# Kernel optimization log

Hardware: AMD Instinct MI355X
Metric: run time of the kernel (lower is better)

The kernel has to match this reference:

```python
import jax, jax.numpy as jnp
import numpy as np

K = 7  # number of relaxed nearest neighbors (init arg k)
EXPM1_GUARD = 1e-7
LOG_HALF = float(np.log(0.5))

def log1mexp(x):
    # log(1 - exp(x)) for x <= 0, numerically stable (guard matches torch bw-path constant)
    t = x < LOG_HALF
    xa = jnp.where(t, x, -1.0)          # safe operand for log1p(-exp(.))
    xb = jnp.where(t, -1.0, x)          # safe operand for log(-expm1(.))
    ya = jnp.log1p(-jnp.exp(xa))
    yb = jnp.log(-jnp.expm1(xb) + EXPM1_GUARD)
    return jnp.where(t, ya, yb)

def setup_inputs() -> dict:
    key = jax.random.key(0)
    k1, k2, k3, k4 = jax.random.split(key, 4)
    b, n, m, o, e, f = 4, 8192, 2048, 64, 64, 128
    x = jax.random.normal(k1, (b, n, f), dtype=jnp.float32)
    xe = jax.random.normal(k2, (b, n, e), dtype=jnp.float32)
    ye = jax.random.normal(k3, (b, m, e), dtype=jnp.float32)
    log_temp_param = jnp.zeros((1,), dtype=jnp.float32)
    I = jax.random.randint(k4, (b, m, o), 0, n, dtype=jnp.int64)
    return {"x": x, "xe": xe, "ye": ye, "log_temp_param": log_temp_param, "I": I}

def reference(x, xe, ye, log_temp_param, I):
    b, n, f = x.shape
    m, o = I.shape[1], I.shape[2]
    bidx = jnp.arange(b)[:, None, None]          # [b,1,1] batch index for gathers

    # ---- compute_distances (indexed path): D[b,m,o] = -||xe[I] - ye||^2 ----
    xg_e = xe[bidx, I]                           # [b,m,o,e] gathered candidate embeddings
    diff = xg_e - ye[:, :, None, :]              # [b,m,o,e]
    D = -jnp.sum(diff * diff, axis=-1)           # [b,m,o]

    # ---- NeuralNearestNeighbors: temperature + k-step relaxed top-k ----
    temperature = jnp.exp(log_temp_param[0])     # log_temp_bias = log(1) = 0
    logits = (D / temperature).reshape(b * m, o)
    samples = []
    for _ in range(K):
        w = jax.nn.log_softmax(logits, axis=1)   # [b*m,o]
        samples.append(jnp.exp(w).reshape(b, m, o))
        logits = logits + log1mexp(w)
    W = jnp.stack(samples, axis=3)               # [b,m,o,K]

    # ---- aggregate_output: z[b,m,f,K] = sum_o W[b,m,o,K] * x[b, I[b,m,o], f] ----
    xg = x[bidx, I]                              # [b,m,o,f]
    z = jnp.einsum('bmok,bmof->bmfk', W, xg)     # [b,m,f,K]
    return z
```

## Files before the change

kernel.cpp:

```cpp
#include <hip/hip_runtime.h>
#include <math.h>

#define B_  4
#define N_  8192
#define M_  2048
#define O_  64
#define E_  64
#define F_  128
#define K_  7

__device__ __forceinline__ unsigned short f32_to_bf16_rne(float f) {
    unsigned u = __float_as_uint(f);
    u += 0x7FFFu + ((u >> 16) & 1u);
    return (unsigned short)(u >> 16);
}

__global__ __launch_bounds__(256) void x_to_bf16_kernel(
    const float* __restrict__ x, unsigned short* __restrict__ xb16)
{
    const size_t i = (size_t)blockIdx.x * 256 + threadIdx.x;
    const float4 v = ((const float4*)x)[i];
    ushort4 o;
    o.x = f32_to_bf16_rne(v.x);
    o.y = f32_to_bf16_rne(v.y);
    o.z = f32_to_bf16_rne(v.z);
    o.w = f32_to_bf16_rne(v.w);
    ((ushort4*)xb16)[i] = o;
}

__global__ __launch_bounds__(128, 6) void n3agg_kernel(
    const unsigned short* __restrict__ xb16, const float* __restrict__ xe,
    const float* __restrict__ ye, const float* __restrict__ log_temp,
    const int* __restrict__ I, float* __restrict__ out)
{
    __shared__ __align__(16) int   s_I[2][O_];
    __shared__ __align__(16) float s_ye[2][E_];
    __shared__ __align__(16) float s_W[2][O_][8];

    const int tid  = threadIdx.x;
    const int w    = tid >> 6;
    const int lane = tid & 63;
    const int bid  = blockIdx.x * 2 + w;
    const int b    = bid >> 11;

    const int my_idx = I[(size_t)bid * O_ + lane];
    s_I[w][lane]  = my_idx;
    s_ye[w][lane] = ye[(size_t)bid * E_ + lane];

    const float4* xr4 = (const float4*)(xe + ((size_t)b * N_ + my_idx) * E_);
    const float4* ye4 = (const float4*)(&s_ye[w][0]);
    float S[16];
    #pragma unroll
    for (int q = 0; q < 4; ++q) {
        float4 xa = xr4[q],      ya = ye4[q];
        float4 xb = xr4[q + 4],  yb = ye4[q + 4];
        float4 xc = xr4[q + 8],  yc = ye4[q + 8];
        float4 xd = xr4[q + 12], yd = ye4[q + 12];
        float da, db, dc, dd;

        da = __fsub_rn(xa.x, ya.x); db = __fsub_rn(xb.x, yb.x);
        dc = __fsub_rn(xc.x, yc.x); dd = __fsub_rn(xd.x, yd.x);
        S[4*q+0] = __fadd_rn(__fadd_rn(__fmul_rn(da,da), __fmul_rn(db,db)),
                             __fadd_rn(__fmul_rn(dc,dc), __fmul_rn(dd,dd)));

        da = __fsub_rn(xa.y, ya.y); db = __fsub_rn(xb.y, yb.y);
        dc = __fsub_rn(xc.y, yc.y); dd = __fsub_rn(xd.y, yd.y);
        S[4*q+1] = __fadd_rn(__fadd_rn(__fmul_rn(da,da), __fmul_rn(db,db)),
                             __fadd_rn(__fmul_rn(dc,dc), __fmul_rn(dd,dd)));

        da = __fsub_rn(xa.z, ya.z); db = __fsub_rn(xb.z, yb.z);
        dc = __fsub_rn(xc.z, yc.z); dd = __fsub_rn(xd.z, yd.z);
        S[4*q+2] = __fadd_rn(__fadd_rn(__fmul_rn(da,da), __fmul_rn(db,db)),
                             __fadd_rn(__fmul_rn(dc,dc), __fmul_rn(dd,dd)));

        da = __fsub_rn(xa.w, ya.w); db = __fsub_rn(xb.w, yb.w);
        dc = __fsub_rn(xc.w, yc.w); dd = __fsub_rn(xd.w, yd.w);
        S[4*q+3] = __fadd_rn(__fadd_rn(__fmul_rn(da,da), __fmul_rn(db,db)),
                             __fadd_rn(__fmul_rn(dc,dc), __fmul_rn(dd,dd)));
    }
    float t8[8], t4[4], t2[2], res;
    #pragma unroll
    for (int l = 0; l < 8; ++l) t8[l] = __fadd_rn(S[l], S[l + 8]);
    #pragma unroll
    for (int l = 0; l < 4; ++l) t4[l] = __fadd_rn(t8[l], t8[l + 4]);
    t2[0] = __fadd_rn(t4[0], t4[2]);
    t2[1] = __fadd_rn(t4[1], t4[3]);
    res   = __fadd_rn(t2[0], t2[1]);

    const float temp = expf(log_temp[0]);
    float logit = __fdiv_rn(-res, temp);

    float wreg[K_];
    #pragma unroll
    for (int k = 0; k < K_; ++k) {
        float mx = logit;
        #pragma unroll
        for (int d = 1; d < 64; d <<= 1) mx = fmaxf(mx, __shfl_xor(mx, d));
        float sh = __fsub_rn(logit, mx);
        float ex = expf(sh);
        float t = __fadd_rn(ex, __shfl_xor(ex, 16));
        t = __fadd_rn(t, __shfl_xor(t, 32));
        t = __fadd_rn(t, __shfl_xor(t, 8));
        t = __fadd_rn(t, __shfl_xor(t, 4));
        t = __fadd_rn(t, __shfl_xor(t, 2));
        t = __fadd_rn(t, __shfl_xor(t, 1));
        const float sm = t;

        float wv = __fsub_rn(sh, logf(sm));
        wreg[k] = expf(wv);

        float lm;
        if (wv < -0.69314718055994530942f) {
            lm = log1pf(-expf(wv));
        } else {
            lm = logf(__fadd_rn(-expm1f(wv), 1e-7f));
        }
        logit = __fadd_rn(logit, lm);
    }
    {
        float* wp = &s_W[w][lane][0];
        *(float4*)wp       = make_float4(wreg[0], wreg[1], wreg[2], wreg[3]);
        *(float2*)(wp + 4) = make_float2(wreg[4], wreg[5]);
        wp[6] = wreg[6];
    }

    const int h  = lane >> 5;
    const int fl = lane & 31;
    float acc[4][K_];
    #pragma unroll
    for (int q = 0; q < 4; ++q)
        #pragma unroll
        for (int k = 0; k < K_; ++k) acc[q][k] = 0.f;

    const unsigned short* xb = xb16 + (size_t)b * N_ * F_ + 4 * fl;
    #pragma unroll 2
    for (int t = 0; t < 32; ++t) {
        const int o = 2 * t + h;
        const int idx = s_I[w][o];
        const ushort4 xu = *(const ushort4*)(xb + (size_t)idx * F_);
        const float xv0 = __uint_as_float((unsigned)xu.x << 16);
        const float xv1 = __uint_as_float((unsigned)xu.y << 16);
        const float xv2 = __uint_as_float((unsigned)xu.z << 16);
        const float xv3 = __uint_as_float((unsigned)xu.w << 16);
        const float* wrow = &s_W[w][o][0];
        const float4 wa = *(const float4*)(wrow);
        const float4 wb = *(const float4*)(wrow + 4);
        const float wk[K_] = {wa.x, wa.y, wa.z, wa.w, wb.x, wb.y, wb.z};
        #pragma unroll
        for (int k = 0; k < K_; ++k) {
            acc[0][k] = fmaf(wk[k], xv0, acc[0][k]);
            acc[1][k] = fmaf(wk[k], xv1, acc[1][k]);
            acc[2][k] = fmaf(wk[k], xv2, acc[2][k]);
            acc[3][k] = fmaf(wk[k], xv3, acc[3][k]);
        }
    }
    #pragma unroll
    for (int q = 0; q < 4; ++q)
        #pragma unroll
        for (int k = 0; k < K_; ++k)
            acc[q][k] += __shfl_xor(acc[q][k], 32);

    if (lane < 32) {
        const float* af = &acc[0][0];
        float4* op4 = (float4*)(out + (size_t)bid * F_ * K_ + fl * 28);
        #pragma unroll
        for (int j = 0; j < 7; ++j)
            op4[j] = make_float4(af[4*j], af[4*j+1], af[4*j+2], af[4*j+3]);
    }
}

__global__ __launch_bounds__(128, 6) void n3agg_fused_f32_kernel(
    const float* __restrict__ x, const float* __restrict__ xe,
    const float* __restrict__ ye, const float* __restrict__ log_temp,
    const int* __restrict__ I, float* __restrict__ out)
{
    __shared__ __align__(16) int   s_I[2][O_];
    __shared__ __align__(16) float s_ye[2][E_];
    __shared__ __align__(16) float s_W[2][O_][8];

    const int tid  = threadIdx.x;
    const int w    = tid >> 6;
    const int lane = tid & 63;
    const int bid  = blockIdx.x * 2 + w;
    const int b    = bid >> 11;

    const int my_idx = I[(size_t)bid * O_ + lane];
    s_I[w][lane]  = my_idx;
    s_ye[w][lane] = ye[(size_t)bid * E_ + lane];

    const float4* xr4 = (const float4*)(xe + ((size_t)b * N_ + my_idx) * E_);
    const float4* ye4 = (const float4*)(&s_ye[w][0]);
    float S[16];
    #pragma unroll
    for (int q = 0; q < 4; ++q) {
        float4 xa = xr4[q],      ya = ye4[q];
        float4 xb = xr4[q + 4],  yb = ye4[q + 4];
        float4 xc = xr4[q + 8],  yc = ye4[q + 8];
        float4 xd = xr4[q + 12], yd = ye4[q + 12];
        float da, db, dc, dd;
        da = __fsub_rn(xa.x, ya.x); db = __fsub_rn(xb.x, yb.x);
        dc = __fsub_rn(xc.x, yc.x); dd = __fsub_rn(xd.x, yd.x);
        S[4*q+0] = __fadd_rn(__fadd_rn(__fmul_rn(da,da), __fmul_rn(db,db)),
                             __fadd_rn(__fmul_rn(dc,dc), __fmul_rn(dd,dd)));
        da = __fsub_rn(xa.y, ya.y); db = __fsub_rn(xb.y, yb.y);
        dc = __fsub_rn(xc.y, yc.y); dd = __fsub_rn(xd.y, yd.y);
        S[4*q+1] = __fadd_rn(__fadd_rn(__fmul_rn(da,da), __fmul_rn(db,db)),
                             __fadd_rn(__fmul_rn(dc,dc), __fmul_rn(dd,dd)));
        da = __fsub_rn(xa.z, ya.z); db = __fsub_rn(xb.z, yb.z);
        dc = __fsub_rn(xc.z, yc.z); dd = __fsub_rn(xd.z, yd.z);
        S[4*q+2] = __fadd_rn(__fadd_rn(__fmul_rn(da,da), __fmul_rn(db,db)),
                             __fadd_rn(__fmul_rn(dc,dc), __fmul_rn(dd,dd)));
        da = __fsub_rn(xa.w, ya.w); db = __fsub_rn(xb.w, yb.w);
        dc = __fsub_rn(xc.w, yc.w); dd = __fsub_rn(xd.w, yd.w);
        S[4*q+3] = __fadd_rn(__fadd_rn(__fmul_rn(da,da), __fmul_rn(db,db)),
                             __fadd_rn(__fmul_rn(dc,dc), __fmul_rn(dd,dd)));
    }
    float t8[8], t4[4], t2[2], res;
    #pragma unroll
    for (int l = 0; l < 8; ++l) t8[l] = __fadd_rn(S[l], S[l + 8]);
    #pragma unroll
    for (int l = 0; l < 4; ++l) t4[l] = __fadd_rn(t8[l], t8[l + 4]);
    t2[0] = __fadd_rn(t4[0], t4[2]);
    t2[1] = __fadd_rn(t4[1], t4[3]);
    res   = __fadd_rn(t2[0], t2[1]);

    const float temp = expf(log_temp[0]);
    float logit = __fdiv_rn(-res, temp);

    float wreg[K_];
    #pragma unroll
    for (int k = 0; k < K_; ++k) {
        float mx = logit;
        #pragma unroll
        for (int d = 1; d < 64; d <<= 1) mx = fmaxf(mx, __shfl_xor(mx, d));
        float sh = __fsub_rn(logit, mx);
        float ex = expf(sh);
        float t = __fadd_rn(ex, __shfl_xor(ex, 16));
        t = __fadd_rn(t, __shfl_xor(t, 32));
        t = __fadd_rn(t, __shfl_xor(t, 8));
        t = __fadd_rn(t, __shfl_xor(t, 4));
        t = __fadd_rn(t, __shfl_xor(t, 2));
        t = __fadd_rn(t, __shfl_xor(t, 1));
        const float sm = t;
        float wv = __fsub_rn(sh, logf(sm));
        wreg[k] = expf(wv);
        float lm;
        if (wv < -0.69314718055994530942f) lm = log1pf(-expf(wv));
        else lm = logf(__fadd_rn(-expm1f(wv), 1e-7f));
        logit = __fadd_rn(logit, lm);
    }
    {
        float* wp = &s_W[w][lane][0];
        *(float4*)wp       = make_float4(wreg[0], wreg[1], wreg[2], wreg[3]);
        *(float2*)(wp + 4) = make_float2(wreg[4], wreg[5]);
        wp[6] = wreg[6];
    }

    const int h  = lane >> 5;
    const int fl = lane & 31;
    float acc[4][K_];
    #pragma unroll
    for (int q = 0; q < 4; ++q)
        #pragma unroll
        for (int k = 0; k < K_; ++k) acc[q][k] = 0.f;
    const float* xb = x + (size_t)b * N_ * F_ + 4 * fl;
    #pragma unroll 2
    for (int t = 0; t < 32; ++t) {
        const int o = 2 * t + h;
        const int idx = s_I[w][o];
        const float4 xv = *(const float4*)(xb + (size_t)idx * F_);
        const float* wrow = &s_W[w][o][0];
        const float4 wa = *(const float4*)(wrow);
        const float4 wb = *(const float4*)(wrow + 4);
        const float wk[K_] = {wa.x, wa.y, wa.z, wa.w, wb.x, wb.y, wb.z};
        #pragma unroll
        for (int k = 0; k < K_; ++k) {
            acc[0][k] = fmaf(wk[k], xv.x, acc[0][k]);
            acc[1][k] = fmaf(wk[k], xv.y, acc[1][k]);
            acc[2][k] = fmaf(wk[k], xv.z, acc[2][k]);
            acc[3][k] = fmaf(wk[k], xv.w, acc[3][k]);
        }
    }
    #pragma unroll
    for (int q = 0; q < 4; ++q)
        #pragma unroll
        for (int k = 0; k < K_; ++k)
            acc[q][k] += __shfl_xor(acc[q][k], 32);
    if (lane < 32) {
        const float* af = &acc[0][0];
        float4* op4 = (float4*)(out + (size_t)bid * F_ * K_ + fl * 28);
        #pragma unroll
        for (int j = 0; j < 7; ++j)
            op4[j] = make_float4(af[4*j], af[4*j+1], af[4*j+2], af[4*j+3]);
    }
}

extern "C" void kernel_launch(void* const* d_in, const int* in_sizes, int n_in,
                              void* d_out, int out_size, void* d_ws, size_t ws_size,
                              hipStream_t stream) {
    const float* x        = (const float*)d_in[0];
    const float* xe       = (const float*)d_in[1];
    const float* ye       = (const float*)d_in[2];
    const float* log_temp = (const float*)d_in[3];
    const int*   I        = (const int*)d_in[4];
    float* out = (float*)d_out;

    const size_t need = (size_t)B_ * N_ * F_ * sizeof(unsigned short);
    if (ws_size >= need) {
        unsigned short* xb16 = (unsigned short*)d_ws;
        hipLaunchKernelGGL(x_to_bf16_kernel,
                           dim3((B_ * N_ * F_) / 4 / 256), dim3(256), 0, stream,
                           x, xb16);
        hipLaunchKernelGGL(n3agg_kernel, dim3((B_ * M_) / 2), dim3(128),
                           0, stream, xb16, xe, ye, log_temp, I, out);
    } else {
        hipLaunchKernelGGL(n3agg_fused_f32_kernel, dim3((B_ * M_) / 2), dim3(128),
                           0, stream, x, xe, ye, log_temp, I, out);
    }
}
```

Before: 68.04 us.

## Warp-specialize each row: one wave computes weights while other prefetches gathered x

Each block now handles a single (b,m) row with two wavefronts. Wave 1 prefetches its half of the gathered bf16 x rows into registers while wave 0 computes distances and the relaxed top-k weights. After a barrier both waves accumulate their halves of o, combine partial sums through shared memory, and write the output cooperatively. Block ids are also remapped across 8 chunks. The change is meant to hide gather latency behind the softmax work, at the cost of doubling the grid, adding barriers, raising register use (launch bounds lowered to 4), and leaving wave 1 idle during the weight phase.

```diff
diff --git a/kernel.cpp b/kernel.cpp
--- a/kernel.cpp
+++ b/kernel.cpp
@@ -28,145 +28,198 @@
     ((ushort4*)xb16)[i] = o;
 }
 
-__global__ __launch_bounds__(128, 6) void n3agg_kernel(
+__global__ __launch_bounds__(128, 4) void n3agg_kernel(
     const unsigned short* __restrict__ xb16, const float* __restrict__ xe,
     const float* __restrict__ ye, const float* __restrict__ log_temp,
     const int* __restrict__ I, float* __restrict__ out)
 {
-    __shared__ __align__(16) int   s_I[2][O_];
-    __shared__ __align__(16) float s_ye[2][E_];
-    __shared__ __align__(16) float s_W[2][O_][8];
+    __shared__ __align__(16) int   s_I[O_];
+    __shared__ __align__(16) float s_ye[E_];
+    __shared__ __align__(16) float s_W[O_][8];
+    __shared__ __align__(16) float s_acc[896];
 
     const int tid  = threadIdx.x;
     const int w    = tid >> 6;
     const int lane = tid & 63;
-    const int bid  = blockIdx.x * 2 + w;
-    const int b    = bid >> 11;
-
-    const int my_idx = I[(size_t)bid * O_ + lane];
-    s_I[w][lane]  = my_idx;
-    s_ye[w][lane] = ye[(size_t)bid * E_ + lane];
-
-    const float4* xr4 = (const float4*)(xe + ((size_t)b * N_ + my_idx) * E_);
-    const float4* ye4 = (const float4*)(&s_ye[w][0]);
-    float S[16];
-    #pragma unroll
-    for (int q = 0; q < 4; ++q) {
-        float4 xa = xr4[q],      ya = ye4[q];
-        float4 xb = xr4[q + 4],  yb = ye4[q + 4];
-        float4 xc = xr4[q + 8],  yc = ye4[q + 8];
-        float4 xd = xr4[q + 12], yd = ye4[q + 12];
-        float da, db, dc, dd;
-
-        da = __fsub_rn(xa.x, ya.x); db = __fsub_rn(xb.x, yb.x);
-        dc = __fsub_rn(xc.x, yc.x); dd = __fsub_rn(xd.x, yd.x);
-        S[4*q+0] = __fadd_rn(__fadd_rn(__fmul_rn(da,da), __fmul_rn(db,db)),
-                             __fadd_rn(__fmul_rn(dc,dc), __fmul_rn(dd,dd)));
-
-        da = __fsub_rn(xa.y, ya.y); db = __fsub_rn(xb.y, yb.y);
-        dc = __fsub_rn(xc.y, yc.y); dd = __fsub_rn(xd.y, yd.y);
-        S[4*q+1] = __fadd_rn(__fadd_rn(__fmul_rn(da,da), __fmul_rn(db,db)),
-                             __fadd_rn(__fmul_rn(dc,dc), __fmul_rn(dd,dd)));
-
-        da = __fsub_rn(xa.z, ya.z); db = __fsub_rn(xb.z, yb.z);
-        dc = __fsub_rn(xc.z, yc.z); dd = __fsub_rn(xd.z, yd.z);
-        S[4*q+2] = __fadd_rn(__fadd_rn(__fmul_rn(da,da), __fmul_rn(db,db)),
-                             __fadd_rn(__fmul_rn(dc,dc), __fmul_rn(dd,dd)));
-
-        da = __fsub_rn(xa.w, ya.w); db = __fsub_rn(xb.w, yb.w);
-        dc = __fsub_rn(xc.w, yc.w); dd = __fsub_rn(xd.w, yd.w);
-        S[4*q+3] = __fadd_rn(__fadd_rn(__fmul_rn(da,da), __fmul_rn(db,db)),
-                             __fadd_rn(__fmul_rn(dc,dc), __fmul_rn(dd,dd)));
-    }
-    float t8[8], t4[4], t2[2], res;
-    #pragma unroll
-    for (int l = 0; l < 8; ++l) t8[l] = __fadd_rn(S[l], S[l + 8]);
-    #pragma unroll
-    for (int l = 0; l < 4; ++l) t4[l] = __fadd_rn(t8[l], t8[l + 4]);
-    t2[0] = __fadd_rn(t4[0], t4[2]);
-    t2[1] = __fadd_rn(t4[1], t4[3]);
-    res   = __fadd_rn(t2[0], t2[1]);
-
-    const float temp = expf(log_temp[0]);
-    float logit = __fdiv_rn(-res, temp);
-
-    float wreg[K_];
-    #pragma unroll
-    for (int k = 0; k < K_; ++k) {
-        float mx = logit;
-        #pragma unroll
-        for (int d = 1; d < 64; d <<= 1) mx = fmaxf(mx, __shfl_xor(mx, d));
-        float sh = __fsub_rn(logit, mx);
-        float ex = expf(sh);
-        float t = __fadd_rn(ex, __shfl_xor(ex, 16));
-        t = __fadd_rn(t, __shfl_xor(t, 32));
-        t = __fadd_rn(t, __shfl_xor(t, 8));
-        t = __fadd_rn(t, __shfl_xor(t, 4));
-        t = __fadd_rn(t, __shfl_xor(t, 2));
-        t = __fadd_rn(t, __shfl_xor(t, 1));
-        const float sm = t;
-
-        float wv = __fsub_rn(sh, logf(sm));
-        wreg[k] = expf(wv);
-
-        float lm;
-        if (wv < -0.69314718055994530942f) {
-            lm = log1pf(-expf(wv));
-        } else {
-            lm = logf(__fadd_rn(-expm1f(wv), 1e-7f));
-        }
-        logit = __fadd_rn(logit, lm);
-    }
-    {
-        float* wp = &s_W[w][lane][0];
+    const int nb    = gridDim.x;
+    const int chunk = nb >> 3;
+    const int blk   = blockIdx.x;
+    const int bid   = (blk & 7) * chunk + (blk >> 3);
+    const int b     = bid >> 11;
+
+    s_I[lane]  = I[(size_t)bid * O_ + lane];
+    s_ye[lane] = ye[(size_t)bid * E_ + lane];
+
+    const int h  = lane >> 5;
+    const int fl = lane & 31;
+    const unsigned short* xb = xb16 + (size_t)b * N_ * F_ + 4 * fl;
+
+    float acc[4][K_];
+    #pragma unroll
+    for (int q = 0; q < 4; ++q)
+        #pragma unroll
+        for (int k = 0; k < K_; ++k) acc[q][k] = 0.f;
+
+    ushort4 xu[16];
+
+    if (w == 1) {
+        #pragma unroll
+        for (int t = 0; t < 16; ++t)
+            xu[t] = *(const ushort4*)(xb + (size_t)s_I[4 * t + 2 * h + 1] * F_);
+    } else {
+        const int my_idx = s_I[lane];
+        const float4* xr4 = (const float4*)(xe + ((size_t)b * N_ + my_idx) * E_);
+        const float4* ye4 = (const float4*)s_ye;
+        float S[16];
+        #pragma unroll
+        for (int q = 0; q < 4; ++q) {
+            float4 xa = xr4[q],      ya = ye4[q];
+            float4 xb2 = xr4[q + 4], yb = ye4[q + 4];
+            float4 xc = xr4[q + 8],  yc = ye4[q + 8];
+            float4 xd = xr4[q + 12], yd = ye4[q + 12];
+            float da, db, dc, dd;
+
+            da = __fsub_rn(xa.x, ya.x); db = __fsub_rn(xb2.x, yb.x);
+            dc = __fsub_rn(xc.x, yc.x); dd = __fsub_rn(xd.x, yd.x);
+            S[4*q+0] = __fadd_rn(__fadd_rn(__fmul_rn(da,da), __fmul_rn(db,db)),
+                                 __fadd_rn(__fmul_rn(dc,dc), __fmul_rn(dd,dd)));
+
+            da = __fsub_rn(xa.y, ya.y); db = __fsub_rn(xb2.y, yb.y);
+            dc = __fsub_rn(xc.y, yc.y); dd = __fsub_rn(xd.y, yd.y);
+            S[4*q+1] = __fadd_rn(__fadd_rn(__fmul_rn(da,da), __fmul_rn(db,db)),
+                                 __fadd_rn(__fmul_rn(dc,dc), __fmul_rn(dd,dd)));
+
+            da = __fsub_rn(xa.z, ya.z); db = __fsub_rn(xb2.z, yb.z);
+            dc = __fsub_rn(xc.z, yc.z); dd = __fsub_rn(xd.z, yd.z);
+            S[4*q+2] = __fadd_rn(__fadd_rn(__fmul_rn(da,da), __fmul_rn(db,db)),
+                                 __fadd_rn(__fmul_rn(dc,dc), __fmul_rn(dd,dd)));
+
+            da = __fsub_rn(xa.w, ya.w); db = __fsub_rn(xb2.w, yb.w);
+            dc = __fsub_rn(xc.w, yc.w); dd = __fsub_rn(xd.w, yd.w);
+            S[4*q+3] = __fadd_rn(__fadd_rn(__fmul_rn(da,da), __fmul_rn(db,db)),
+                                 __fadd_rn(__fmul_rn(dc,dc), __fmul_rn(dd,dd)));
+        }
+        float t8[8], t4[4], t2[2], res;
+        #pragma unroll
+        for (int l = 0; l < 8; ++l) t8[l] = __fadd_rn(S[l], S[l + 8]);
+        #pragma unroll
+        for (int l = 0; l < 4; ++l) t4[l] = __fadd_rn(t8[l], t8[l + 4]);
+        t2[0] = __fadd_rn(t4[0], t4[2]);
+        t2[1] = __fadd_rn(t4[1], t4[3]);
+        res   = __fadd_rn(t2[0], t2[1]);
+
+        const float temp = expf(log_temp[0]);
+        float logit = __fdiv_rn(-res, temp);
+
+        float wreg[K_];
+        #pragma unroll
+        for (int k = 0; k < K_; ++k) {
+            float mx = logit;
+            #pragma unroll
+            for (int d = 1; d < 64; d <<= 1) mx = fmaxf(mx, __shfl_xor(mx, d));
+            float sh = __fsub_rn(logit, mx);
+            float ex = expf(sh);
+            float t = __fadd_rn(ex, __shfl_xor(ex, 16));
+            t = __fadd_rn(t, __shfl_xor(t, 32));
+            t = __fadd_rn(t, __shfl_xor(t, 8));
+            t = __fadd_rn(t, __shfl_xor(t, 4));
+            t = __fadd_rn(t, __shfl_xor(t, 2));
+            t = __fadd_rn(t, __shfl_xor(t, 1));
+            const float sm = t;
+
+            float wv = __fsub_rn(sh, logf(sm));
+            wreg[k] = expf(wv);
+
+            float lm;
+            if (wv < -0.69314718055994530942f) {
+                lm = log1pf(-expf(wv));
+            } else {
+                lm = logf(__fadd_rn(-expm1f(wv), 1e-7f));
+            }
+            logit = __fadd_rn(logit, lm);
+        }
+        float* wp = &s_W[lane][0];
         *(float4*)wp       = make_float4(wreg[0], wreg[1], wreg[2], wreg[3]);
         *(float2*)(wp + 4) = make_float2(wreg[4], wreg[5]);
         wp[6] = wreg[6];
     }
 
-    const int h  = lane >> 5;
-    const int fl = lane & 31;
-    float acc[4][K_];
-    #pragma unroll
-    for (int q = 0; q < 4; ++q)
-        #pragma unroll
-        for (int k = 0; k < K_; ++k) acc[q][k] = 0.f;
-
-    const unsigned short* xb = xb16 + (size_t)b * N_ * F_ + 4 * fl;
-    #pragma unroll 2
-    for (int t = 0; t < 32; ++t) {
-        const int o = 2 * t + h;
-        const int idx = s_I[w][o];
-        const ushort4 xu = *(const ushort4*)(xb + (size_t)idx * F_);
-        const float xv0 = __uint_as_float((unsigned)xu.x << 16);
-        const float xv1 = __uint_as_float((unsigned)xu.y << 16);
-        const float xv2 = __uint_as_float((unsigned)xu.z << 16);
-        const float xv3 = __uint_as_float((unsigned)xu.w << 16);
-        const float* wrow = &s_W[w][o][0];
-        const float4 wa = *(const float4*)(wrow);
-        const float4 wb = *(const float4*)(wrow + 4);
-        const float wk[K_] = {wa.x, wa.y, wa.z, wa.w, wb.x, wb.y, wb.z};
-        #pragma unroll
-        for (int k = 0; k < K_; ++k) {
-            acc[0][k] = fmaf(wk[k], xv0, acc[0][k]);
-            acc[1][k] = fmaf(wk[k], xv1, acc[1][k]);
-            acc[2][k] = fmaf(wk[k], xv2, acc[2][k]);
-            acc[3][k] = fmaf(wk[k], xv3, acc[3][k]);
-        }
-    }
+    __syncthreads();
+
+    if (w == 1) {
+        #pragma unroll
+        for (int t = 0; t < 16; ++t) {
+            const int o = 4 * t + 2 * h + 1;
+            const float xv0 = __uint_as_float((unsigned)xu[t].x << 16);
+            const float xv1 = __uint_as_float((unsigned)xu[t].y << 16);
+            const float xv2 = __uint_as_float((unsigned)xu[t].z << 16);
+            const float xv3 = __uint_as_float((unsigned)xu[t].w << 16);
+            const float* wr = &s_W[o][0];
+            const float4 wa = *(const float4*)(wr);
+            const float4 wb = *(const float4*)(wr + 4);
+            const float wk[K_] = {wa.x, wa.y, wa.z, wa.w, wb.x, wb.y, wb.z};
+            #pragma unroll
+            for (int k = 0; k < K_; ++k) {
+                acc[0][k] = fmaf(wk[k], xv0, acc[0][k]);
+                acc[1][k] = fmaf(wk[k], xv1, acc[1][k]);
+                acc[2][k] = fmaf(wk[k], xv2, acc[2][k]);
+                acc[3][k] = fmaf(wk[k], xv3, acc[3][k]);
+            }
+        }
+    } else {
+        ushort4 xv[16];
+        #pragma unroll
+        for (int t = 0; t < 16; ++t)
+            xv[t] = *(const ushort4*)(xb + (size_t)s_I[4 * t + 2 * h] * F_);
+        #pragma unroll
+        for (int t = 0; t < 16; ++t) {
+            const int o = 4 * t + 2 * h;
+            const float xv0 = __uint_as_float((unsigned)xv[t].x << 16);
+            const float xv1 = __uint_as_float((unsigned)xv[t].y << 16);
+            const float xv2 = __uint_as_float((unsigned)xv[t].z << 16);
+            const float xv3 = __uint_as_float((unsigned)xv[t].w << 16);
+            const float* wr = &s_W[o][0];
+            const float4 wa = *(const float4*)(wr);
+            const float4 wb = *(const float4*)(wr + 4);
+            const float wk[K_] = {wa.x, wa.y, wa.z, wa.w, wb.x, wb.y, wb.z};
+            #pragma unroll
+            for (int k = 0; k < K_; ++k) {
+                acc[0][k] = fmaf(wk[k], xv0, acc[0][k]);
+                acc[1][k] = fmaf(wk[k], xv1, acc[1][k]);
+                acc[2][k] = fmaf(wk[k], xv2, acc[2][k]);
+                acc[3][k] = fmaf(wk[k], xv3, acc[3][k]);
+            }
+        }
+    }
+
     #pragma unroll
     for (int q = 0; q < 4; ++q)
         #pragma unroll
         for (int k = 0; k < K_; ++k)
             acc[q][k] += __shfl_xor(acc[q][k], 32);
 
-    if (lane < 32) {
+    if (w == 1 && lane < 32) {
         const float* af = &acc[0][0];
-        float4* op4 = (float4*)(out + (size_t)bid * F_ * K_ + fl * 28);
+        float* so = &s_acc[fl * 28];
         #pragma unroll
         for (int j = 0; j < 7; ++j)
-            op4[j] = make_float4(af[4*j], af[4*j+1], af[4*j+2], af[4*j+3]);
-    }
+            *(float4*)(so + 4 * j) = make_float4(af[4*j], af[4*j+1],
+                                                 af[4*j+2], af[4*j+3]);
+    }
+    __syncthreads();
+    if (w == 0 && lane < 32) {
+        const float* af = &acc[0][0];
+        float* so = &s_acc[fl * 28];
+        #pragma unroll
+        for (int j = 0; j < 28; ++j)
+            so[j] += af[j];
+    }
+    __syncthreads();
+
+    const float4* sp = (const float4*)s_acc;
+    float4* ob = (float4*)(out + (size_t)bid * (F_ * K_));
+    ob[tid] = sp[tid];
+    if (tid < 96) ob[tid + 128] = sp[tid + 128];
 }
 
 __global__ __launch_bounds__(128, 6) void n3agg_fused_f32_kernel(
@@ -311,7 +364,7 @@
         hipLaunchKernelGGL(x_to_bf16_kernel,
                            dim3((B_ * N_ * F_) / 4 / 256), dim3(256), 0, stream,
                            x, xb16);
-        hipLaunchKernelGGL(n3agg_kernel, dim3((B_ * M_) / 2), dim3(128),
+        hipLaunchKernelGGL(n3agg_kernel, dim3(B_ * M_), dim3(128),
                            0, stream, xb16, xe, ye, log_temp, I, out);
     } else {
         hipLaunchKernelGGL(n3agg_fused_f32_kernel, dim3((B_ * M_) / 2), dim3(128),
```

Measured after the change: 84.31 us. +23.9%, slower.

## Double-buffer bf16 gathers and swizzle block order across XCDs

Applied to the files above, without the earlier changes.

The aggregation loop now prefetches the next four gathered bf16 rows of x into registers while the FMAs run on the current four, so gather latency overlaps with compute. Block indices are also remapped so that consecutive hardware block IDs, which are spread round-robin over the 8 XCDs, land on contiguous chunks of rows. That should keep batch-local gathers in the same XCD's L2. The price is higher register pressure from the extra ushort4 buffers, and the remap assumes the grid size is divisible by 8.

```diff
diff --git a/kernel.cpp b/kernel.cpp
--- a/kernel.cpp
+++ b/kernel.cpp
@@ -40,8 +40,12 @@
     const int tid  = threadIdx.x;
     const int w    = tid >> 6;
     const int lane = tid & 63;
-    const int bid  = blockIdx.x * 2 + w;
-    const int b    = bid >> 11;
+    const int nb    = gridDim.x;
+    const int chunk = nb >> 3;
+    const int blk   = blockIdx.x;
+    const int sb    = (blk & 7) * chunk + (blk >> 3);
+    const int bid   = sb * 2 + w;
+    const int b     = bid >> 11;
 
     const int my_idx = I[(size_t)bid * O_ + lane];
     s_I[w][lane]  = my_idx;
@@ -133,27 +137,46 @@
         for (int k = 0; k < K_; ++k) acc[q][k] = 0.f;
 
     const unsigned short* xb = xb16 + (size_t)b * N_ * F_ + 4 * fl;
-    #pragma unroll 2
-    for (int t = 0; t < 32; ++t) {
-        const int o = 2 * t + h;
-        const int idx = s_I[w][o];
-        const ushort4 xu = *(const ushort4*)(xb + (size_t)idx * F_);
-        const float xv0 = __uint_as_float((unsigned)xu.x << 16);
-        const float xv1 = __uint_as_float((unsigned)xu.y << 16);
-        const float xv2 = __uint_as_float((unsigned)xu.z << 16);
-        const float xv3 = __uint_as_float((unsigned)xu.w << 16);
-        const float* wrow = &s_W[w][o][0];
-        const float4 wa = *(const float4*)(wrow);
-        const float4 wb = *(const float4*)(wrow + 4);
-        const float wk[K_] = {wa.x, wa.y, wa.z, wa.w, wb.x, wb.y, wb.z};
-        #pragma unroll
-        for (int k = 0; k < K_; ++k) {
-            acc[0][k] = fmaf(wk[k], xv0, acc[0][k]);
-            acc[1][k] = fmaf(wk[k], xv1, acc[1][k]);
-            acc[2][k] = fmaf(wk[k], xv2, acc[2][k]);
-            acc[3][k] = fmaf(wk[k], xv3, acc[3][k]);
+    ushort4 bufA[4], bufB[4];
+    #pragma unroll
+    for (int j = 0; j < 4; ++j)
+        bufA[j] = *(const ushort4*)(xb + (size_t)s_I[w][2 * j + h] * F_);
+
+    #pragma unroll
+    for (int g = 0; g < 8; ++g) {
+        if (g < 7) {
+            if ((g & 1) == 0) {
+                #pragma unroll
+                for (int j = 0; j < 4; ++j)
+                    bufB[j] = *(const ushort4*)(xb + (size_t)s_I[w][2*((g+1)*4+j) + h] * F_);
+            } else {
+                #pragma unroll
+                for (int j = 0; j < 4; ++j)
+                    bufA[j] = *(const ushort4*)(xb + (size_t)s_I[w][2*((g+1)*4+j) + h] * F_);
+            }
         }
-    }
+        #pragma unroll
+        for (int j = 0; j < 4; ++j) {
+            const ushort4 xu = ((g & 1) == 0) ? bufA[j] : bufB[j];
+            const int o = 2 * (g * 4 + j) + h;
+            const float xv0 = __uint_as_float((unsigned)xu.x << 16);
+            const float xv1 = __uint_as_float((unsigned)xu.y << 16);
+            const float xv2 = __uint_as_float((unsigned)xu.z << 16);
+            const float xv3 = __uint_as_float((unsigned)xu.w << 16);
+            const float* wrow = &s_W[w][o][0];
+            const float4 wa = *(const float4*)(wrow);
+            const float4 wb = *(const float4*)(wrow + 4);
+            const float wk[K_] = {wa.x, wa.y, wa.z, wa.w, wb.x, wb.y, wb.z};
+            #pragma unroll
+            for (int k = 0; k < K_; ++k) {
+                acc[0][k] = fmaf(wk[k], xv0, acc[0][k]);
+                acc[1][k] = fmaf(wk[k], xv1, acc[1][k]);
+                acc[2][k] = fmaf(wk[k], xv2, acc[2][k]);
+                acc[3][k] = fmaf(wk[k], xv3, acc[3][k]);
+            }
+        }
+    }
+
     #pragma unroll
     for (int q = 0; q < 4; ++q)
         #pragma unroll
```

After: 170.2 us. 150% more time.
